# Kernel optimization log

Measured on AMD Instinct MI355X. Metric: run time of the kernel, lower is better.

Reference implementation:

```python
import jax, jax.numpy as jnp
import numpy as np

N, D, H, K, P = 1536, 1024, 16, 64, 8
FREQ_DIM = 14 * 3 * 128  # freq_embedding(pos, 128) flattened


def freq_embedding(t, size):
    # min_freq=0.01, max_freq=2**8 as in the block's call sites
    nf = size // 2
    freqs = (2.0 ** jnp.linspace(np.log2(0.01), np.log2(256.0), nf)).astype(jnp.float32)
    r = t[..., None] * freqs
    return jnp.stack((jnp.sin(r), jnp.cos(r)), axis=-1).reshape(t.shape[0], -1)


def layer_norm(x, eps=1e-5):
    m = jnp.mean(x, -1, keepdims=True)
    v = jnp.var(x, -1, keepdims=True)
    return (x - m) * jax.lax.rsqrt(v + eps)


def cond_norm(x, cond, ws, bs, wb, bb):
    return jax.nn.sigmoid(cond @ ws + bs) * layer_norm(x) + (cond @ wb + bb)


def _unit(v):
    return v * jax.lax.rsqrt(jnp.sum(v * v, -1, keepdims=True) + 1e-8)


def aa_frames(pos):
    # Gram-Schmidt frame from backbone N/CA/C (atom14 slots 0,1,2)
    n, ca, c = pos[:, 0], pos[:, 1], pos[:, 2]
    e1 = _unit(c - ca)
    v2 = n - ca
    e2 = _unit(v2 - jnp.sum(e1 * v2, -1, keepdims=True) * e1)
    e3 = jnp.cross(e1, e2)
    R = jnp.stack([e1, e2, e3], axis=-1)  # [N,3,3]
    return R, ca


def setup_inputs():
    key = jax.random.key(0)
    ks = iter(jax.random.split(key, 64))
    r = lambda *s: jax.random.normal(next(ks), s, jnp.float32)
    w = lambda *s: 0.02 * jax.random.normal(next(ks), s, jnp.float32)
    z = lambda *s: jnp.zeros(s, jnp.float32)
    return dict(
        local=r(N, D), pos=r(N, 14, 3), condition=r(N, D),
        mask=jnp.ones((N,), bool), pair_bias=r(H, N, N),
        w_f1=w(FREQ_DIM, 2 * D), b_f1=z(2 * D), w_f2=w(2 * D, D), b_f2=z(D),
        cn1_ws=w(D, D), cn1_bs=z(D), cn1_wb=w(D, D), cn1_bb=z(D),
        wq=w(D, H * K), wk=w(D, H * K), wv=w(D, H * K),
        wqp=w(D, H * P * 3), wkp=w(D, H * P * 3), wvp=w(D, H * P * 3),
        gamma=z(H), wo=w(H * (K + 4 * P), D), bo=z(D),
        cn2_ws=w(D, D), cn2_bs=z(D), cn2_wb=w(D, D), cn2_bb=z(D),
        wg1=w(D, 2 * D), bg1=z(2 * D), wg2=w(D, 2 * D), bg2=z(2 * D),
        wg3=w(2 * D, D), bg3=z(D),
        cn3_ws=w(D, D), cn3_bs=z(D), cn3_wb=w(D, D), cn3_bb=z(D),
        w_vel=w(D, 14 * 3),
    )


def reference(local, pos, condition, mask, pair_bias,
              w_f1, b_f1, w_f2, b_f2,
              cn1_ws, cn1_bs, cn1_wb, cn1_bb,
              wq, wk, wv, wqp, wkp, wvp, gamma, wo, bo,
              cn2_ws, cn2_bs, cn2_wb, cn2_bb,
              wg1, bg1, wg2, bg2, wg3, bg3,
              cn3_ws, cn3_bs, cn3_wb, cn3_bb, w_vel):
    n = local.shape[0]
    # embed_pred_pos: MLP over freq embedding of coords
    emb = freq_embedding(pos, 128)  # [N, 5376]
    local = local + (jax.nn.silu(emb @ w_f1 + b_f1) @ w_f2 + b_f2)
    # attention branch
    ai = cond_norm(local, condition, cn1_ws, cn1_bs, cn1_wb, cn1_bb)
    R, t = aa_frames(pos)
    q = (ai @ wq).reshape(n, H, K)
    k = (ai @ wk).reshape(n, H, K)
    v = (ai @ wv).reshape(n, H, K)
    to_glob = lambda p: jnp.einsum('nab,nhpb->nhpa', R, p) + t[:, None, None, :]
    qg = to_glob((ai @ wqp).reshape(n, H, P, 3))
    kg = to_glob((ai @ wkp).reshape(n, H, P, 3))
    vg = to_glob((ai @ wvp).reshape(n, H, P, 3))
    qk = jnp.einsum('ihk,jhk->hij', q, k) / np.sqrt(K).astype(np.float32)
    # squared point distances via norm expansion (never materialize [H,N,N,P,3])
    ptdot = jnp.einsum('ihpc,jhpc->hij', qg, kg)
    qn = jnp.sum(qg * qg, axis=(-1, -2)).T  # [H,N]
    kn = jnp.sum(kg * kg, axis=(-1, -2)).T
    dist2 = qn[:, :, None] + kn[None if False else slice(None), None, :] - 2.0 * ptdot
    wc = np.sqrt(2.0 / (9.0 * P)).astype(np.float32)
    logits = qk + pair_bias - 0.5 * wc * jax.nn.softplus(gamma)[:, None, None] * dist2
    logits = jnp.where(mask[None, None, :], logits, -1e9)
    a = jax.nn.softmax(logits, axis=-1)  # [H,N,N]
    o = jnp.einsum('hij,jhk->ihk', a, v).reshape(n, H * K)
    opg = jnp.einsum('hij,jhpc->ihpc', a, vg)
    opl = jnp.einsum('nba,nhpb->nhpa', R, opg - t[:, None, None, :])
    onorm = jnp.sqrt(jnp.sum(opl * opl, -1) + 1e-8).reshape(n, -1)
    upd = jnp.concatenate([o, opl.reshape(n, -1), onorm], axis=-1) @ wo + bo
    local = local + upd
    # gated MLP branch
    x = cond_norm(local, condition, cn2_ws, cn2_bs, cn2_wb, cn2_bb)
    local = local + (jax.nn.silu(x @ wg1 + bg1) * (x @ wg2 + bg2)) @ wg3 + bg3
    # output heads
    ln = cond_norm(local, condition, cn3_ws, cn3_bs, cn3_wb, cn3_bb)
    velocity = (ln @ w_vel).reshape(n, 14, 3)
    return local, velocity
```

## Files before the change

### kernel.cpp

```cpp
#include <hip/hip_runtime.h>
#include <hip/hip_bf16.h>
#include <math.h>

#define NRES 1536
#define NH 16
#define NNF 2359296ull
#define LOG2E 1.44269504f
#define KVS 4
#define LDQ 4224
#define NTPJ 19

typedef unsigned short u16;
typedef __attribute__((ext_vector_type(8))) short short8;
typedef __attribute__((ext_vector_type(4))) unsigned short u16x4;
typedef __attribute__((ext_vector_type(4))) float f32x4;

typedef const __attribute__((address_space(1))) void gvoid;
typedef __attribute__((address_space(3))) void lvoid;

__device__ __forceinline__ u16 f2b(float x){
    __hip_bfloat16 h = __float2bfloat16(x);
    return *reinterpret_cast<u16*>(&h);
}
__device__ __forceinline__ float b2f(u16 u){
    unsigned v = ((unsigned)u) << 16;
    return __uint_as_float(v);
}

#define F_BIAS  1
#define F_SILU  2
#define F_RESID 8
#define F_OUTBF 16

template<int TNF>
__global__ __launch_bounds__(256) void gemm_t(
    const u16* __restrict__ A, int lda, size_t zsA,
    const u16* __restrict__ BT, int ldb, size_t zsB,
    float* __restrict__ Cf, u16* __restrict__ Cb, int ldc, size_t zsC,
    const float* __restrict__ bias, size_t zsBias,
    const float* __restrict__ resid, int ldr, size_t zsR,
    int Ncols, int Kd, int flags, int ksl)
{
    constexpr int TN = TNF * 32;
    __shared__ u16 As[2][128 * 64];
    __shared__ u16 Bs[2][TN * 64];

    unsigned gx = gridDim.x, gy = gridDim.y;
    unsigned nb = gx * gy * gridDim.z;
    unsigned bid = (blockIdx.z * gy + blockIdx.y) * gx + blockIdx.x;
    if ((nb & 7u) == 0u) bid = (bid & 7u) * (nb >> 3) + (bid >> 3);
    const int bxi = bid % gx;
    const int byi = (bid / gx) % gy;
    const int bz  = bid / (gx * gy);

    const int tid = threadIdx.x;
    const int l = tid & 63, w = tid >> 6;
    const int bm = byi * 128, bn = bxi * TN;

    A  += zsA * bz;
    BT += zsB * bz;

    const int kbeg = ksl ? bz * ksl : 0;
    const int kend = ksl ? kbeg + ksl : Kd;
    const int nk = (kend - kbeg) >> 6;

    const int arow   = l >> 3;
    const int aslot  = l & 7;
    const int srcslt = aslot ^ arow;

    const u16* aBase[4];
    const u16* bBase[TN / 32];
    #pragma unroll
    for (int t = 0; t < 4; ++t) {
        int ra = bm + (w * 4 + t) * 8 + arow;
        aBase[t] = A + (size_t)ra * lda + srcslt * 8;
    }
    #pragma unroll
    for (int t = 0; t < TN / 32; ++t) {
        int rb = bn + (w * (TN / 32) + t) * 8 + arow;
        if (rb > Ncols - 1) rb = Ncols - 1;
        bBase[t] = BT + (size_t)rb * ldb + srcslt * 8;
    }

    const int wr = w >> 1, wc = w & 1;
    const int fr = l & 15;
    const int fq = l >> 4;

    f32x4 acc[4][TNF];
    #pragma unroll
    for (int i = 0; i < 4; ++i)
        #pragma unroll
        for (int j = 0; j < TNF; ++j) acc[i][j] = (f32x4){0.f, 0.f, 0.f, 0.f};

    auto stage = [&](int buf, int k0) {
        #pragma unroll
        for (int t = 0; t < 4; ++t)
            __builtin_amdgcn_global_load_lds((gvoid*)(aBase[t] + k0),
                (lvoid*)((char*)As[buf] + (w * 4 + t) * 1024), 16, 0, 0);
        #pragma unroll
        for (int t = 0; t < TN / 32; ++t)
            __builtin_amdgcn_global_load_lds((gvoid*)(bBase[t] + k0),
                (lvoid*)((char*)Bs[buf] + (w * (TN / 32) + t) * 1024), 16, 0, 0);
    };

    stage(0, kbeg);
    __syncthreads();
    int cur = 0;

    for (int it = 0; it < nk; ++it) {
        if (it + 1 < nk) stage(cur ^ 1, kbeg + (it + 1) * 64);
        #pragma unroll
        for (int kk = 0; kk < 2; ++kk) {
            const int slotR = ((kk * 4) + fq) ^ (l & 7);
            short8 av[4], bv[TNF];
            #pragma unroll
            for (int m = 0; m < 4; ++m) {
                int r = wr * 64 + m * 16 + fr;
                av[m] = *(const short8*)((const char*)As[cur] + r * 128 + slotR * 16);
            }
            #pragma unroll
            for (int n = 0; n < TNF; ++n) {
                int r = wc * (TNF * 16) + n * 16 + fr;
                bv[n] = *(const short8*)((const char*)Bs[cur] + r * 128 + slotR * 16);
            }
            #pragma unroll
            for (int m = 0; m < 4; ++m)
                #pragma unroll
                for (int n = 0; n < TNF; ++n)
                    acc[m][n] = __builtin_amdgcn_mfma_f32_16x16x32_bf16(av[m], bv[n], acc[m][n], 0, 0, 0);
        }
        __syncthreads();
        cur ^= 1;
    }

    const float* residz = (flags & F_RESID) ? resid + zsR * bz : nullptr;
    const float* biasz  = (flags & F_BIAS)  ? bias + zsBias * bz : nullptr;
    float* cfz = Cf ? Cf + zsC * bz : nullptr;
    u16*   cbz = Cb ? Cb + zsC * bz : nullptr;

    #pragma unroll
    for (int m = 0; m < 4; ++m) {
        #pragma unroll
        for (int n = 0; n < TNF; ++n) {
            int gc = bn + wc * (TNF * 16) + n * 16 + fr;
            if (gc >= Ncols) continue;
            int gr0 = bm + wr * 64 + m * 16 + fq * 4;
            #pragma unroll
            for (int r = 0; r < 4; ++r) {
                int gr = gr0 + r;
                float v = acc[m][n][r];
                if (flags & F_BIAS)  v += biasz[gc];
                if (flags & F_SILU)  v = v / (1.f + expf(-v));
                if (flags & F_RESID) v += residz[(size_t)gr * ldr + gc];
                if (flags & F_OUTBF) cbz[(size_t)gr * ldc + gc] = f2b(v);
                else                 cfz[(size_t)gr * ldc + gc] = v;
            }
        }
    }
}

__global__ __launch_bounds__(256) void reduce_epi(
    const u16* __restrict__ part, size_t slice, int nsl,
    float* __restrict__ Cf, u16* __restrict__ Cb,
    const float* __restrict__ bias,
    const float* __restrict__ resid, int ldr,
    int M, int Ncols, int flags)
{
    if ((Ncols & 7) == 0) {
        size_t total8 = (size_t)M * Ncols / 8;
        for (size_t i8 = (size_t)blockIdx.x * 256 + threadIdx.x; i8 < total8;
             i8 += (size_t)gridDim.x * 256) {
            size_t i0 = i8 * 8;
            int r = (int)(i0 / (unsigned)Ncols);
            int c0 = (int)(i0 - (size_t)r * Ncols);
            float v[8] = {0,0,0,0,0,0,0,0};
            for (int s = 0; s < nsl; ++s) {
                const u16x4* p = (const u16x4*)(part + (size_t)s * slice + i0);
                u16x4 a = p[0], b = p[1];
                v[0] += b2f(a.x); v[1] += b2f(a.y); v[2] += b2f(a.z); v[3] += b2f(a.w);
                v[4] += b2f(b.x); v[5] += b2f(b.y); v[6] += b2f(b.z); v[7] += b2f(b.w);
            }
            #pragma unroll
            for (int j = 0; j < 8; ++j) {
                if (flags & F_BIAS) v[j] += bias[c0 + j];
                if (flags & F_SILU) v[j] = v[j] / (1.f + expf(-v[j]));
            }
            if (flags & F_RESID) {
                const float4* rp = (const float4*)(resid + (size_t)r * ldr + c0);
                float4 r0 = rp[0], r1 = rp[1];
                v[0] += r0.x; v[1] += r0.y; v[2] += r0.z; v[3] += r0.w;
                v[4] += r1.x; v[5] += r1.y; v[6] += r1.z; v[7] += r1.w;
            }
            if (flags & F_OUTBF) {
                short8 o;
                #pragma unroll
                for (int j = 0; j < 8; ++j) o[j] = (short)f2b(v[j]);
                *(short8*)(Cb + i0) = o;
            } else {
                float4 o0 = {v[0], v[1], v[2], v[3]}, o1 = {v[4], v[5], v[6], v[7]};
                float4* cp = (float4*)(Cf + i0);
                cp[0] = o0; cp[1] = o1;
            }
        }
    } else {
        size_t total = (size_t)M * Ncols;
        for (size_t i = (size_t)blockIdx.x * 256 + threadIdx.x; i < total;
             i += (size_t)gridDim.x * 256) {
            float v = 0.f;
            for (int s = 0; s < nsl; ++s) v += b2f(part[(size_t)s * slice + i]);
            if (flags & F_OUTBF) Cb[i] = f2b(v);
            else                 Cf[i] = v;
        }
    }
}

__global__ __launch_bounds__(256) void reduce_cn(
    const u16* __restrict__ part, size_t slice, int nsl,
    const float* __restrict__ bias, const float* __restrict__ resid,
    float* __restrict__ locOut,
    const u16* __restrict__ cs, const u16* __restrict__ cb,
    u16* __restrict__ normB)
{
    int row = blockIdx.x, tid = threadIdx.x;
    size_t base = (size_t)row * 1024 + tid * 4;
    float v[4];
    {
        float4 rv = *(const float4*)(resid + base);
        v[0] = rv.x; v[1] = rv.y; v[2] = rv.z; v[3] = rv.w;
    }
    for (int s = 0; s < nsl; ++s) {
        u16x4 p = *(const u16x4*)(part + (size_t)s * slice + base);
        v[0] += b2f(p.x); v[1] += b2f(p.y); v[2] += b2f(p.z); v[3] += b2f(p.w);
    }
    {
        float4 bv = *(const float4*)(bias + tid * 4);
        v[0] += bv.x; v[1] += bv.y; v[2] += bv.z; v[3] += bv.w;
    }
    *(float4*)(locOut + base) = (float4){v[0], v[1], v[2], v[3]};

    float s1 = v[0] + v[1] + v[2] + v[3];
    float s2 = v[0]*v[0] + v[1]*v[1] + v[2]*v[2] + v[3]*v[3];
    __shared__ float r1[256], r2[256];
    r1[tid] = s1; r2[tid] = s2;
    __syncthreads();
    for (int st = 128; st > 0; st >>= 1) {
        if (tid < st) { r1[tid] += r1[tid + st]; r2[tid] += r2[tid + st]; }
        __syncthreads();
    }
    float mean = r1[0] * (1.f / 1024.f);
    float var = r2[0] * (1.f / 1024.f) - mean * mean;
    float rs = rsqrtf(var + 1e-5f);
    u16x4 sv = *(const u16x4*)(cs + base);
    u16x4 bv = *(const u16x4*)(cb + base);
    u16x4 o;
    o.x = f2b((1.f / (1.f + expf(-b2f(sv.x)))) * (v[0] - mean) * rs + b2f(bv.x));
    o.y = f2b((1.f / (1.f + expf(-b2f(sv.y)))) * (v[1] - mean) * rs + b2f(bv.y));
    o.z = f2b((1.f / (1.f + expf(-b2f(sv.z)))) * (v[2] - mean) * rs + b2f(bv.z));
    o.w = f2b((1.f / (1.f + expf(-b2f(sv.w)))) * (v[3] - mean) * rs + b2f(bv.w));
    *(u16x4*)(normB + base) = o;
}

__global__ __launch_bounds__(256, 2) void attn_kernel(
    const u16* __restrict__ qe, const u16* __restrict__ ke,
    const u16* __restrict__ vt, const float* __restrict__ pb,
    u16* __restrict__ Opart, float* __restrict__ mlpart)
{
    __shared__ u16 Ks[2][64 * 128];
    __shared__ u16 Vs[2][96 * 64];
    __shared__ u16 Ps[64 * 64];

    unsigned gx = gridDim.x, gy = gridDim.y;
    unsigned nb = gx * gy * gridDim.z;
    unsigned bid = (blockIdx.z * gy + blockIdx.y) * gx + blockIdx.x;
    bid = (bid & 7u) * (nb >> 3) + (bid >> 3);
    const int qx = bid % gx;
    const int h  = (bid / gx) % gy;
    const int z  = bid / (gx * gy);

    const int tid = threadIdx.x;
    const int l = tid & 63, w = tid >> 6;
    const int q0 = qx * 64;
    const int fr = l & 15, fq = l >> 4;

    const u16* keh = ke + (size_t)h * NRES * 128;
    const u16* vth = vt + (size_t)h * 96 * NRES;

    const int kr4 = l >> 4, ks16 = l & 15;
    const int vr8 = l >> 3, vs8 = l & 7;

    short8 qv[4];
    {
        const u16* qrow = qe + ((size_t)h * NRES + (q0 + w * 16 + fr)) * 128 + fq * 8;
        #pragma unroll
        for (int kk = 0; kk < 4; ++kk)
            qv[kk] = *(const short8*)(qrow + kk * 32);
    }

    float m_run[4], l_run[4];
    f32x4 oacc[6];
    #pragma unroll
    for (int r = 0; r < 4; ++r) { m_run[r] = -1e30f; l_run[r] = 0.f; }
    #pragma unroll
    for (int n = 0; n < 6; ++n) oacc[n] = (f32x4){0.f, 0.f, 0.f, 0.f};

    const int NIT = NRES / 64 / KVS;
    const int jbase = z * (NRES / KVS);
    int cur = 0;

    auto stage = [&](int buf, int j0) {
        #pragma unroll
        for (int t = 0; t < 4; ++t) {
            int row = w * 16 + t * 4 + kr4;
            int ss = ks16 ^ (row & 7);
            __builtin_amdgcn_global_load_lds(
                (gvoid*)(keh + (size_t)(j0 + row) * 128 + ss * 8),
                (lvoid*)((char*)Ks[buf] + (w * 16 + t * 4) * 256), 16, 0, 0);
        }
        #pragma unroll
        for (int t = 0; t < 3; ++t) {
            int row = w * 24 + t * 8 + vr8;
            int ss = vs8 ^ (row & 7);
            __builtin_amdgcn_global_load_lds(
                (gvoid*)(vth + (size_t)row * NRES + j0 + ss * 8),
                (lvoid*)((char*)Vs[buf] + (w * 24 + t * 8) * 128), 16, 0, 0);
        }
    };
    const float* pbrow = pb + ((size_t)h * NRES + (q0 + w * 16 + fq * 4)) * NRES + fr;

    f32x4 pbv[4], pbn[4] = {};
    stage(0, jbase);
    #pragma unroll
    for (int n = 0; n < 4; ++n)
        #pragma unroll
        for (int r = 0; r < 4; ++r)
            pbv[n][r] = pbrow[(size_t)r * NRES + jbase + n * 16];
    __syncthreads();

    for (int it = 0; it < NIT; ++it) {
        if (it + 1 < NIT) {
            int j1 = jbase + (it + 1) * 64;
            stage(cur ^ 1, j1);
            #pragma unroll
            for (int n = 0; n < 4; ++n)
                #pragma unroll
                for (int r = 0; r < 4; ++r)
                    pbn[n][r] = pbrow[(size_t)r * NRES + j1 + n * 16];
        }

        f32x4 sacc[4];
        #pragma unroll
        for (int n = 0; n < 4; ++n) sacc[n] = (f32x4){0.f, 0.f, 0.f, 0.f};
        __builtin_amdgcn_s_setprio(1);
        #pragma unroll
        for (int kk = 0; kk < 4; ++kk) {
            #pragma unroll
            for (int n = 0; n < 4; ++n) {
                int row = n * 16 + fr;
                short8 bv = *(const short8*)((const char*)Ks[cur] + row * 256
                                             + (((kk * 4 + fq) ^ (fr & 7)) * 16));
                sacc[n] = __builtin_amdgcn_mfma_f32_16x16x32_bf16(qv[kk], bv, sacc[n], 0, 0, 0);
            }
        }
        __builtin_amdgcn_s_setprio(0);
        #pragma unroll
        for (int n = 0; n < 4; ++n) sacc[n] += pbv[n];

        float alpha[4];
        #pragma unroll
        for (int r = 0; r < 4; ++r) {
            float v = fmaxf(fmaxf(sacc[0][r], sacc[1][r]), fmaxf(sacc[2][r], sacc[3][r]));
            v = fmaxf(v, __shfl_xor(v, 1, 64));
            v = fmaxf(v, __shfl_xor(v, 2, 64));
            v = fmaxf(v, __shfl_xor(v, 4, 64));
            v = fmaxf(v, __shfl_xor(v, 8, 64));
            float mn = fmaxf(m_run[r], v);
            alpha[r] = exp2f((m_run[r] - mn) * LOG2E);
            m_run[r] = mn;
        }

        float psum[4] = {0.f, 0.f, 0.f, 0.f};
        #pragma unroll
        for (int n = 0; n < 4; ++n) {
            int col = n * 16 + fr;
            #pragma unroll
            for (int r = 0; r < 4; ++r) {
                float p = exp2f((sacc[n][r] - m_run[r]) * LOG2E);
                psum[r] += p;
                int rowf = w * 16 + fq * 4 + r;
                int byte = rowf * 128 + (((col >> 3) ^ (rowf & 7)) * 16) + (col & 7) * 2;
                *(u16*)((char*)Ps + byte) = f2b(p);
            }
        }
        #pragma unroll
        for (int r = 0; r < 4; ++r) {
            float v = psum[r];
            v += __shfl_xor(v, 1, 64);
            v += __shfl_xor(v, 2, 64);
            v += __shfl_xor(v, 4, 64);
            v += __shfl_xor(v, 8, 64);
            l_run[r] = l_run[r] * alpha[r] + v;
        }
        #pragma unroll
        for (int n = 0; n < 6; ++n)
            #pragma unroll
            for (int r = 0; r < 4; ++r)
                oacc[n][r] *= alpha[r];

        __builtin_amdgcn_s_setprio(1);
        #pragma unroll
        for (int kk = 0; kk < 2; ++kk) {
            int prow = w * 16 + fr;
            short8 pa = *(const short8*)((const char*)Ps + prow * 128
                                         + (((kk * 4 + fq) ^ (prow & 7)) * 16));
            #pragma unroll
            for (int n = 0; n < 6; ++n) {
                int vrow = n * 16 + fr;
                short8 vv = *(const short8*)((const char*)Vs[cur] + vrow * 128
                                             + (((kk * 4 + fq) ^ (fr & 7)) * 16));
                oacc[n] = __builtin_amdgcn_mfma_f32_16x16x32_bf16(pa, vv, oacc[n], 0, 0, 0);
            }
        }
        __builtin_amdgcn_s_setprio(0);

        __syncthreads();
        cur ^= 1;
        #pragma unroll
        for (int n = 0; n < 4; ++n) pbv[n] = pbn[n];
    }

    u16* Oz = Opart + ((size_t)z * NH + h) * NRES * 96;
    #pragma unroll
    for (int n = 0; n < 6; ++n) {
        int c = n * 16 + fr;
        #pragma unroll
        for (int r = 0; r < 4; ++r) {
            int row = q0 + w * 16 + fq * 4 + r;
            Oz[(size_t)row * 96 + c] = f2b(oacc[n][r]);
        }
    }
    if (fr == 0) {
        float* mlz = mlpart + ((size_t)z * NH + h) * NRES * 2;
        #pragma unroll
        for (int r = 0; r < 4; ++r) {
            int row = q0 + w * 16 + fq * 4 + r;
            mlz[row * 2 + 0] = m_run[r];
            mlz[row * 2 + 1] = l_run[r];
        }
    }
}

__global__ __launch_bounds__(256) void combine_fin(
    const u16* __restrict__ Opart, const float* __restrict__ mlpart,
    const float* __restrict__ Rb, const float* __restrict__ tb,
    u16* __restrict__ featB)
{
    int idx = blockIdx.x * 256 + threadIdx.x;
    if (idx >= NRES * NH) return;
    int n = idx >> 4, h = idx & 15;

    float m[KVS], lv[KVS], wgt[KVS];
    float mm = -1e30f;
    #pragma unroll
    for (int s = 0; s < KVS; ++s) {
        size_t rr = ((size_t)s * NH + h) * NRES + n;
        m[s] = mlpart[rr * 2];
        lv[s] = mlpart[rr * 2 + 1];
        mm = fmaxf(mm, m[s]);
    }
    float ll = 0.f;
    #pragma unroll
    for (int s = 0; s < KVS; ++s) {
        wgt[s] = exp2f((m[s] - mm) * LOG2E);
        ll += lv[s] * wgt[s];
    }
    float inv = 1.f / ll;
    const u16* op[KVS];
    #pragma unroll
    for (int s = 0; s < KVS; ++s)
        op[s] = Opart + (((size_t)s * NH + h) * NRES + n) * 96;

    u16* fb = featB + (size_t)n * 1536;
    #pragma unroll
    for (int k = 0; k < 64; ++k) {
        float v = 0.f;
        #pragma unroll
        for (int s = 0; s < KVS; ++s) v += b2f(op[s][k]) * wgt[s];
        fb[h * 64 + k] = f2b(v * inv);
    }

    float R[9];
    #pragma unroll
    for (int a = 0; a < 9; ++a) R[a] = Rb[(size_t)n * 9 + a];
    float t0 = tb[(size_t)n * 3 + 0], t1 = tb[(size_t)n * 3 + 1], t2 = tb[(size_t)n * 3 + 2];
    #pragma unroll
    for (int p = 0; p < 8; ++p) {
        float d[3];
        #pragma unroll
        for (int dd = 0; dd < 3; ++dd) {
            int c = 64 + p * 3 + dd;
            float v = 0.f;
            #pragma unroll
            for (int s = 0; s < KVS; ++s) v += b2f(op[s][c]) * wgt[s];
            d[dd] = v * inv;
        }
        float x = d[0] - t0, y = d[1] - t1, z = d[2] - t2;
        float a0 = R[0] * x + R[3] * y + R[6] * z;
        float a1 = R[1] * x + R[4] * y + R[7] * z;
        float a2 = R[2] * x + R[5] * y + R[8] * z;
        fb[1024 + h * 24 + p * 3 + 0] = f2b(a0);
        fb[1024 + h * 24 + p * 3 + 1] = f2b(a1);
        fb[1024 + h * 24 + p * 3 + 2] = f2b(a2);
        fb[1408 + h * 8 + p] = f2b(sqrtf(a0 * a0 + a1 * a1 + a2 * a2 + 1e-8f));
    }
}

struct TpMega {
    const float* src[NTPJ];
    u16* dst[NTPJ];
    int ldi[NTPJ], ldo[NTPJ], K[NTPJ], N[NTPJ];
    int bx[NTPJ], start[NTPJ];
};

__global__ __launch_bounds__(256) void transpose_mega(TpMega J)
{
    __shared__ float t[32][33];
    int b = blockIdx.x;
    int j = NTPJ - 1;
    while (J.start[j] > b) --j;
    int lb = b - J.start[j];
    int bxn = J.bx[j];
    int n0 = (lb % bxn) * 32;
    int k0 = (lb / bxn) * 32;
    const float* in = J.src[j];
    u16* out = J.dst[j];
    int ldi = J.ldi[j], ldo = J.ldo[j], Kk = J.K[j], Nn = J.N[j];
    int tx = threadIdx.x & 31, ty = threadIdx.x >> 5;
    #pragma unroll
    for (int jj = 0; jj < 4; ++jj) {
        int k = k0 + ty + jj * 8;
        if (k < Kk && n0 + tx < Nn) t[ty + jj * 8][tx] = in[(size_t)k * ldi + n0 + tx];
    }
    __syncthreads();
    #pragma unroll
    for (int jj = 0; jj < 4; ++jj) {
        int n = n0 + ty + jj * 8;
        int k = k0 + tx;
        if (n < Nn && k < Kk) out[(size_t)n * ldo + k] = f2b(t[tx][ty + jj * 8]);
    }
}

__global__ __launch_bounds__(256) void vt_pack(
    const float* __restrict__ qkc, const float* __restrict__ vgt,
    u16* __restrict__ vt)
{
    __shared__ float t[32][33];
    int h = blockIdx.z, grp = blockIdx.y, n0 = blockIdx.x * 32;
    int tx = threadIdx.x & 31, ty = threadIdx.x >> 5;
    #pragma unroll
    for (int j = 0; j < 4; ++j) {
        int n = n0 + ty + j * 8;
        int c = grp * 32 + tx;
        float v = 0.f;
        if (c < 64) v = qkc[(size_t)n * LDQ + 2048 + h * 64 + c];
        else if (c < 88) v = vgt[(size_t)n * 384 + h * 24 + (c - 64)];
        t[ty + j * 8][tx] = v;
    }
    __syncthreads();
    #pragma unroll
    for (int j = 0; j < 4; ++j) {
        int r = grp * 32 + ty + j * 8;
        vt[((size_t)h * 96 + r) * NRES + n0 + tx] = f2b(t[tx][ty + j * 8]);
    }
}

__global__ __launch_bounds__(256) void prologue_kernel(
    const float* __restrict__ pos, const float* __restrict__ cond,
    const float* __restrict__ cn1_bs, const float* __restrict__ cn1_bb,
    const float* __restrict__ cn2_bs, const float* __restrict__ cn2_bb,
    const float* __restrict__ cn3_bs, const float* __restrict__ cn3_bb,
    const float* __restrict__ bg1, const float* __restrict__ bg2,
    float* __restrict__ Rb, float* __restrict__ tb,
    u16* __restrict__ emb, u16* __restrict__ condB,
    float* __restrict__ bias2, float* __restrict__ biasg)
{
    int b = blockIdx.x, tid = threadIdx.x;
    if (b < 16128) {
        int idx = b * 256 + tid;
        int f = idx & 63;
        int rest = idx >> 6;
        int coord = rest % 42;
        int n = rest / 42;
        float t = pos[(size_t)n * 42 + coord];
        const double l0 = -6.643856189774724;
        const double step = 14.643856189774724 / 63.0;
        float freq = exp2f((float)(l0 + f * step));
        float r = t * freq;
        size_t o = (size_t)n * 5376 + (size_t)coord * 128 + 2 * f;
        emb[o]     = f2b(sinf(r));
        emb[o + 1] = f2b(cosf(r));
    } else if (b < 16896) {
        int i = (b - 16128) * 256 + tid;
        size_t i0 = (size_t)i * 8;
        const float4* p = (const float4*)(cond + i0);
        float4 a = p[0], bb = p[1];
        short8 o;
        o[0]=(short)f2b(a.x); o[1]=(short)f2b(a.y); o[2]=(short)f2b(a.z); o[3]=(short)f2b(a.w);
        o[4]=(short)f2b(bb.x); o[5]=(short)f2b(bb.y); o[6]=(short)f2b(bb.z); o[7]=(short)f2b(bb.w);
        *(short8*)(condB + i0) = o;
    } else if (b < 16902) {
        int n = (b - 16896) * 256 + tid;
        if (n >= NRES) return;
        const float* p = pos + (size_t)n * 42;
        float nx = p[0], ny = p[1], nz = p[2];
        float cax = p[3], cay = p[4], caz = p[5];
        float cx = p[6], cy = p[7], cz = p[8];
        float v1x = cx - cax, v1y = cy - cay, v1z = cz - caz;
        float i1 = rsqrtf(v1x * v1x + v1y * v1y + v1z * v1z + 1e-8f);
        float e1x = v1x * i1, e1y = v1y * i1, e1z = v1z * i1;
        float v2x = nx - cax, v2y = ny - cay, v2z = nz - caz;
        float d = e1x * v2x + e1y * v2y + e1z * v2z;
        float wx = v2x - d * e1x, wy = v2y - d * e1y, wz = v2z - d * e1z;
        float i2 = rsqrtf(wx * wx + wy * wy + wz * wz + 1e-8f);
        float e2x = wx * i2, e2y = wy * i2, e2z = wz * i2;
        float e3x = e1y * e2z - e1z * e2y;
        float e3y = e1z * e2x - e1x * e2z;
        float e3z = e1x * e2y - e1y * e2x;
        float* R = Rb + (size_t)n * 9;
        R[0] = e1x; R[1] = e2x; R[2] = e3x;
        R[3] = e1y; R[4] = e2y; R[5] = e3y;
        R[6] = e1z; R[7] = e2z; R[8] = e3z;
        tb[(size_t)n * 3 + 0] = cax;
        tb[(size_t)n * 3 + 1] = cay;
        tb[(size_t)n * 3 + 2] = caz;
    } else if (b < 16906) {
        int i = (b - 16902) * 256 + tid;
        if (i >= 1024) return;
        bias2[i] = cn1_bs[i]; bias2[1024 + i] = cn1_bb[i]; bias2[2048 + i] = cn2_bs[i];
        bias2[3072 + i] = cn2_bb[i]; bias2[4096 + i] = cn3_bs[i]; bias2[5120 + i] = cn3_bb[i];
    } else {
        int i = (b - 16906) * 256 + tid;
        if (i >= 2048) return;
        biasg[i] = bg1[i]; biasg[2048 + i] = bg2[i];
    }
}

__global__ __launch_bounds__(256) void pack_attn(
    const float* __restrict__ qkc,
    const float* __restrict__ Rb, const float* __restrict__ tb,
    const float* __restrict__ gamma,
    u16* __restrict__ qe, u16* __restrict__ ke, float* __restrict__ vgt)
{
    int b = blockIdx.x;
    if (b < 1536) {
        int idx = b * 256 + threadIdx.x;
        int g = idx & 15;
        int t = idx >> 4;
        int n = t % NRES;
        int h = t / NRES;
        size_t o = ((size_t)h * NRES + n) * 128 + g * 8;
        if (g < 8) {
            const float4* q4 = (const float4*)(qkc + (size_t)n * LDQ + h * 64 + g * 8);
            const float4* k4 = (const float4*)(qkc + (size_t)n * LDQ + 1024 + h * 64 + g * 8);
            float4 qa = q4[0], qb2 = q4[1], ka = k4[0], kb2 = k4[1];
            short8 oq, ok;
            oq[0]=(short)f2b(0.125f*qa.x); oq[1]=(short)f2b(0.125f*qa.y);
            oq[2]=(short)f2b(0.125f*qa.z); oq[3]=(short)f2b(0.125f*qa.w);
            oq[4]=(short)f2b(0.125f*qb2.x); oq[5]=(short)f2b(0.125f*qb2.y);
            oq[6]=(short)f2b(0.125f*qb2.z); oq[7]=(short)f2b(0.125f*qb2.w);
            ok[0]=(short)f2b(ka.x); ok[1]=(short)f2b(ka.y); ok[2]=(short)f2b(ka.z); ok[3]=(short)f2b(ka.w);
            ok[4]=(short)f2b(kb2.x); ok[5]=(short)f2b(kb2.y); ok[6]=(short)f2b(kb2.z); ok[7]=(short)f2b(kb2.w);
            *(short8*)(qe + o) = oq;
            *(short8*)(ke + o) = ok;
        } else if (g >= 11) {
            short8 zz = {};
            *(short8*)(qe + o) = zz;
            *(short8*)(ke + o) = zz;
        }
        return;
    }
    int idx = (b - 1536) * 256 + threadIdx.x;
    if (idx >= NRES * NH) return;
    int n = idx >> 4, h = idx & 15;
    float R[9];
    #pragma unroll
    for (int a = 0; a < 9; ++a) R[a] = Rb[(size_t)n * 9 + a];
    float t0 = tb[(size_t)n * 3 + 0], t1 = tb[(size_t)n * 3 + 1], t2 = tb[(size_t)n * 3 + 2];
    float g = gamma[h];
    float sp = (g > 20.f) ? g : log1pf(expf(g));
    float ch = 0.5f * (1.f / 6.f) * sp;

    u16* qeh = qe + ((size_t)h * NRES + n) * 128;
    u16* keh = ke + ((size_t)h * NRES + n) * 128;
    const float* qp = qkc + (size_t)n * LDQ + 3072 + h * 24;
    const float* kp = qkc + (size_t)n * LDQ + 3456 + h * 24;
    const float* vp = qkc + (size_t)n * LDQ + 3840 + h * 24;
    float kn = 0.f;
    #pragma unroll
    for (int p = 0; p < 8; ++p) {
        {
            float x = qp[p*3], y = qp[p*3+1], z = qp[p*3+2];
            float g0 = R[0] * x + R[1] * y + R[2] * z + t0;
            float g1 = R[3] * x + R[4] * y + R[5] * z + t1;
            float g2 = R[6] * x + R[7] * y + R[8] * z + t2;
            qeh[64 + p * 3 + 0] = f2b(2.f * ch * g0);
            qeh[64 + p * 3 + 1] = f2b(2.f * ch * g1);
            qeh[64 + p * 3 + 2] = f2b(2.f * ch * g2);
        }
        {
            float x = kp[p*3], y = kp[p*3+1], z = kp[p*3+2];
            float g0 = R[0] * x + R[1] * y + R[2] * z + t0;
            float g1 = R[3] * x + R[4] * y + R[5] * z + t1;
            float g2 = R[6] * x + R[7] * y + R[8] * z + t2;
            keh[64 + p * 3 + 0] = f2b(g0);
            keh[64 + p * 3 + 1] = f2b(g1);
            keh[64 + p * 3 + 2] = f2b(g2);
            kn += g0 * g0 + g1 * g1 + g2 * g2;
        }
        {
            float x = vp[p*3], y = vp[p*3+1], z = vp[p*3+2];
            vgt[(size_t)n * 384 + h * 24 + p * 3 + 0] = R[0] * x + R[1] * y + R[2] * z + t0;
            vgt[(size_t)n * 384 + h * 24 + p * 3 + 1] = R[3] * x + R[4] * y + R[5] * z + t1;
            vgt[(size_t)n * 384 + h * 24 + p * 3 + 2] = R[6] * x + R[7] * y + R[8] * z + t2;
        }
    }
    qeh[88] = f2b(1.0f);
    keh[88] = f2b(-ch * kn);
}

__global__ __launch_bounds__(256) void glu_kernel(const u16* __restrict__ g12, u16* __restrict__ gm)
{
    int i = blockIdx.x * 256 + threadIdx.x;
    if (i >= NRES * 2048 / 8) return;
    size_t i0 = (size_t)i * 8;
    short8 a8 = *(const short8*)(g12 + i0);
    short8 b8 = *(const short8*)(g12 + (size_t)NRES * 2048 + i0);
    short8 o;
    #pragma unroll
    for (int j = 0; j < 8; ++j) {
        float a = b2f((u16)a8[j]);
        float b = b2f((u16)b8[j]);
        float s = a / (1.f + expf(-a));
        o[j] = (short)f2b(s * b);
    }
    *(short8*)(gm + i0) = o;
}

extern "C" void kernel_launch(void* const* d_in, const int* in_sizes, int n_in,
                              void* d_out, int out_size, void* d_ws, size_t ws_size,
                              hipStream_t stream)
{
    const float* local_in = (const float*)d_in[0];
    const float* pos      = (const float*)d_in[1];
    const float* cond     = (const float*)d_in[2];
    const float* pb       = (const float*)d_in[4];
    const float* w_f1     = (const float*)d_in[5];
    const float* b_f1     = (const float*)d_in[6];
    const float* w_f2     = (const float*)d_in[7];
    const float* b_f2     = (const float*)d_in[8];
    const float* cn1_ws   = (const float*)d_in[9];
    const float* cn1_bs   = (const float*)d_in[10];
    const float* cn1_wb   = (const float*)d_in[11];
    const float* cn1_bb   = (const float*)d_in[12];
    const float* wq       = (const float*)d_in[13];
    const float* wk       = (const float*)d_in[14];
    const float* wv       = (const float*)d_in[15];
    const float* wqp      = (const float*)d_in[16];
    const float* wkp      = (const float*)d_in[17];
    const float* wvp      = (const float*)d_in[18];
    const float* gamma    = (const float*)d_in[19];
    const float* wo       = (const float*)d_in[20];
    const float* bo       = (const float*)d_in[21];
    const float* cn2_ws   = (const float*)d_in[22];
    const float* cn2_bs   = (const float*)d_in[23];
    const float* cn2_wb   = (const float*)d_in[24];
    const float* cn2_bb   = (const float*)d_in[25];
    const float* wg1      = (const float*)d_in[26];
    const float* bg1      = (const float*)d_in[27];
    const float* wg2      = (const float*)d_in[28];
    const float* bg2      = (const float*)d_in[29];
    const float* wg3      = (const float*)d_in[30];
    const float* bg3      = (const float*)d_in[31];
    const float* cn3_ws   = (const float*)d_in[32];
    const float* cn3_bs   = (const float*)d_in[33];
    const float* cn3_wb   = (const float*)d_in[34];
    const float* cn3_bb   = (const float*)d_in[35];
    const float* w_vel    = (const float*)d_in[36];

    float* out = (float*)d_out;
    float* ws  = (float*)d_ws;

    size_t off = 0;
    auto alloc = [&](size_t nf) -> float* { float* p = ws + off; off += (nf + 7) & ~7ull; return p; };

    const size_t NN1 = (size_t)NRES * 1024;
    float* Rb    = alloc(NRES * 9);
    float* tb    = alloc(NRES * 3);
    float* loc   = alloc(NN1);
    u16*   cs6b  = (u16*)alloc(6 * NN1 / 2);
    u16*   condB = (u16*)alloc(NN1 / 2);
    u16*   normB = (u16*)alloc(NN1 / 2);
    float* bias2 = alloc(6 * 1024);
    float* biasg = alloc(2 * 2048);
    float* qkc   = alloc((size_t)NRES * LDQ);
    float* vgt   = alloc((size_t)NRES * 384);
    u16*   qeB   = (u16*)alloc((size_t)NH * NRES * 128 / 2);
    u16*   keB   = (u16*)alloc((size_t)NH * NRES * 128 / 2);
    u16*   vTB   = (u16*)alloc((size_t)NH * 96 * NRES / 2);
    u16*   featB = (u16*)alloc((size_t)NRES * 1536 / 2);
    u16*   g1sB  = (u16*)alloc((size_t)NRES * 2048 / 2);
    u16*   gmB   = (u16*)alloc((size_t)NRES * 2048 / 2);
    u16*   cnT9  = (u16*)alloc((size_t)9 * 1024 * 1024 / 2);
    u16*   ptsT  = (u16*)alloc((size_t)3 * 384 * 1024 / 2);
    u16*   wgT   = (u16*)alloc((size_t)2 * 2048 * 1024 / 2);
    u16*   wf1T  = (u16*)alloc((size_t)2048 * 5376 / 2);
    u16*   wf2T  = (u16*)alloc((size_t)1024 * 2048 / 2);
    u16*   woT   = (u16*)alloc((size_t)1024 * 1536 / 2);
    u16*   wg3T  = (u16*)alloc((size_t)1024 * 2048 / 2);
    u16*   wvT   = (u16*)alloc((size_t)42 * 1024 / 2 + 8);
    u16*   embB  = (u16*)alloc((size_t)NRES * 5376 / 2);
    u16*   hidB  = (u16*)alloc((size_t)NRES * 2048 / 2);
    u16*   pscr  = (u16*)alloc((size_t)2 * NRES * 2048 * 4 / 2);
    u16*   Opart = (u16*)alloc((size_t)KVS * NH * NRES * 96 / 2);
    float* mlprt = alloc((size_t)KVS * NH * NRES * 2);

    const float* nilf = nullptr;

    auto gemm = [&](int tnf, const u16* A, int lda, size_t zsA,
                    const u16* BT, int ldb, size_t zsB,
                    float* Cf, u16* Cb2, int ldc, size_t zsC,
                    const float* bias, size_t zsBias,
                    const float* resid, int ldr, size_t zsR,
                    int Nc, int Kd, int flags, int gz, int ksl) {
        int tn = tnf * 32;
        dim3 grid((Nc + tn - 1) / tn, NRES / 128, gz);
        if (tnf == 4)
            hipLaunchKernelGGL(gemm_t<4>, grid, dim3(256), 0, stream,
                               A, lda, zsA, BT, ldb, zsB, Cf, Cb2, ldc, zsC,
                               bias, zsBias, resid, ldr, zsR, Nc, Kd, flags, ksl);
        else
            hipLaunchKernelGGL(gemm_t<2>, grid, dim3(256), 0, stream,
                               A, lda, zsA, BT, ldb, zsB, Cf, Cb2, ldc, zsC,
                               bias, zsBias, resid, ldr, zsR, Nc, Kd, flags, ksl);
    };
    auto red = [&](const u16* part, size_t slice, int nsl, float* Cf, u16* Cb2,
                   const float* bias, const float* resid, int ldr, int Nc, int flags) {
        hipLaunchKernelGGL(reduce_epi, dim3(1024), dim3(256), 0, stream,
                           part, slice, nsl, Cf, Cb2, bias, resid, ldr, NRES, Nc, flags);
    };
    auto redcn = [&](const u16* part, size_t slice, int nsl,
                     const float* bias, const float* resid, float* locOut, int cnIdx) {
        hipLaunchKernelGGL(reduce_cn, dim3(NRES), dim3(256), 0, stream,
                           part, slice, nsl, bias, resid, locOut,
                           cs6b + (size_t)(2 * cnIdx) * NN1,
                           cs6b + (size_t)(2 * cnIdx + 1) * NN1, normB);
    };

    hipLaunchKernelGGL(prologue_kernel, dim3(16914), dim3(256), 0, stream,
                       pos, cond, cn1_bs, cn1_bb, cn2_bs, cn2_bb, cn3_bs, cn3_bb,
                       bg1, bg2, Rb, tb, embB, condB, bias2, biasg);

    {
        TpMega J;
        int jn = 0, start = 0;
        auto addJob = [&](const float* src, u16* dst, int ldi, int ldo, int K, int N) {
            J.src[jn] = src; J.dst[jn] = dst;
            J.ldi[jn] = ldi; J.ldo[jn] = ldo; J.K[jn] = K; J.N[jn] = N;
            int bx = (N + 31) / 32, by = (K + 31) / 32;
            J.bx[jn] = bx; J.start[jn] = start;
            start += bx * by;
            ++jn;
        };
        const float* cn6[6] = {cn1_ws, cn1_wb, cn2_ws, cn2_wb, cn3_ws, cn3_wb};
        for (int i = 0; i < 6; ++i)
            addJob(cn6[i], cnT9 + (size_t)i * 1024 * 1024, 1024, 1024, 1024, 1024);
        addJob(wq, cnT9 + (size_t)6 * 1024 * 1024, 1024, 1024, 1024, 1024);
        addJob(wk, cnT9 + (size_t)7 * 1024 * 1024, 1024, 1024, 1024, 1024);
        addJob(wv, cnT9 + (size_t)8 * 1024 * 1024, 1024, 1024, 1024, 1024);
        addJob(wqp, ptsT,                        384, 1024, 1024, 384);
        addJob(wkp, ptsT + (size_t)384 * 1024,   384, 1024, 1024, 384);
        addJob(wvp, ptsT + (size_t)2 * 384 * 1024, 384, 1024, 1024, 384);
        addJob(wg1, wgT,                        2048, 1024, 1024, 2048);
        addJob(wg2, wgT + (size_t)2048 * 1024,  2048, 1024, 1024, 2048);
        addJob(w_f1, wf1T, 2048, 5376, 5376, 2048);
        addJob(w_f2, wf2T, 1024, 2048, 2048, 1024);
        addJob(wo,   woT,  1024, 1536, 1536, 1024);
        addJob(wg3,  wg3T, 1024, 2048, 2048, 1024);
        addJob(w_vel, wvT,   42, 1024, 1024, 42);
        hipLaunchKernelGGL(transpose_mega, dim3(start), dim3(256), 0, stream, J);
    }

    gemm(2, condB, 1024, 0, cnT9, 1024, (size_t)1024 * 1024, nullptr, cs6b, 1024, NN1,
         bias2, 1024, nilf, 0, 0, 1024, 1024, F_BIAS | F_OUTBF, 6, 0);

    gemm(2, embB, 5376, 0, wf1T, 5376, 0, nullptr, pscr, 2048, (size_t)NRES * 2048,
         nilf, 0, nilf, 0, 0, 2048, 5376, F_OUTBF, 4, 1344);
    red(pscr, (size_t)NRES * 2048, 4, nullptr, hidB, b_f1, nilf, 0,
        2048, F_BIAS | F_SILU | F_OUTBF);
    gemm(2, hidB, 2048, 0, wf2T, 2048, 0, nullptr, pscr, 1024, NN1,
         nilf, 0, nilf, 0, 0, 1024, 2048, F_OUTBF, 4, 512);
    redcn(pscr, NN1, 4, b_f2, local_in, loc, 0);

    gemm(2, normB, 1024, 0, cnT9 + (size_t)6 * 1024 * 1024, 1024, 0,
         qkc, nullptr, LDQ, 0, nilf, 0, nilf, 0, 0, LDQ, 1024, 0, 1, 0);

    hipLaunchKernelGGL(pack_attn, dim3(1536 + 96), dim3(256), 0, stream,
                       qkc, Rb, tb, gamma, qeB, keB, vgt);
    hipLaunchKernelGGL(vt_pack, dim3(NRES / 32, 3, NH), dim3(256), 0, stream,
                       qkc, vgt, vTB);

    hipLaunchKernelGGL(attn_kernel, dim3(NRES / 64, NH, KVS), dim3(256), 0, stream,
                       qeB, keB, vTB, pb, Opart, mlprt);
    hipLaunchKernelGGL(combine_fin, dim3(96), dim3(256), 0, stream,
                       Opart, mlprt, Rb, tb, featB);

    gemm(2, featB, 1536, 0, woT, 1536, 0, nullptr, pscr, 1024, NN1,
         nilf, 0, nilf, 0, 0, 1024, 1536, F_OUTBF, 4, 384);
    redcn(pscr, NN1, 4, bo, loc, loc, 1);

    gemm(2, normB, 1024, 0, wgT, 1024, (size_t)2048 * 1024, nullptr, g1sB, 2048, (size_t)NRES * 2048,
         biasg, 2048, nilf, 0, 0, 2048, 1024, F_BIAS | F_OUTBF, 2, 0);
    u16* gmO = embB;
    hipLaunchKernelGGL(glu_kernel, dim3((NRES * 2048 / 8 + 255) / 256), dim3(256), 0, stream, g1sB, gmO);
    gemm(2, gmO, 2048, 0, wg3T, 2048, 0, nullptr, pscr, 1024, NN1,
         nilf, 0, nilf, 0, 0, 1024, 2048, F_OUTBF, 4, 512);
    redcn(pscr, NN1, 4, bg3, loc, out, 2);

    gemm(2, normB, 1024, 0, wvT, 1024, 0, nullptr, pscr, 42, (size_t)NRES * 42,
         nilf, 0, nilf, 0, 0, 42, 1024, F_OUTBF, 8, 128);
    red(pscr, (size_t)NRES * 42, 8, out + (size_t)NRES * 1024, nullptr,
        nilf, nilf, 0, 42, 0);
}
```

Measured before the change: 464.7 us.

## Merge prologue with weight transposes and batch two independent GEMMs in one launch

Folds the weight-transpose blocks into the prologue kernel as extra blocks, and replaces two back-to-back GEMM launches (condition-projection GEMM and split-K freq-embedding GEMM) with a single dual-job GEMM kernel that dispatches blocks by index. This removes launch gaps and tail underutilization between small independent kernels so their blocks can co-schedule. The dual kernel uses a fixed 128x64 tile and its own block swizzle, which may differ in efficiency from the original templated gemm. The shared-memory tile is now allocated for every prologue block, which may reduce occupancy of the embedding blocks.

```diff
diff --git a/kernel.cpp b/kernel.cpp
--- a/kernel.cpp
+++ b/kernel.cpp
@@ -9,6 +9,7 @@
 #define KVS 4
 #define LDQ 4224
 #define NTPJ 19
+#define PROBLK 16914
 
 typedef unsigned short u16;
 typedef __attribute__((ext_vector_type(8))) short short8;
@@ -154,6 +155,130 @@
                 if (flags & F_RESID) v += residz[(size_t)gr * ldr + gc];
                 if (flags & F_OUTBF) cbz[(size_t)gr * ldc + gc] = f2b(v);
                 else                 cfz[(size_t)gr * ldc + gc] = v;
+            }
+        }
+    }
+}
+
+struct GJob {
+    const u16* A;
+    const u16* BT;
+    u16* C;
+    const float* bias;
+    int lda, ldb, ldc;
+    size_t zsA, zsB, zsC, zsBias;
+    int Nc, Kd, ksl, flags;
+    unsigned gx, gy, start, nb;
+};
+
+__global__ __launch_bounds__(256) void gemm_dual(GJob j0, GJob j1)
+{
+    __shared__ u16 As[2][128 * 64];
+    __shared__ u16 Bs[2][64 * 64];
+
+    GJob J = (blockIdx.x >= j1.start) ? j1 : j0;
+    unsigned bid = blockIdx.x - J.start;
+    if ((J.nb & 7u) == 0u) bid = (bid & 7u) * (J.nb >> 3) + (bid >> 3);
+    const int bxi = bid % J.gx;
+    const int byi = (bid / J.gx) % J.gy;
+    const int bz  = bid / (J.gx * J.gy);
+
+    const int tid = threadIdx.x;
+    const int l = tid & 63, w = tid >> 6;
+    const int bm = byi * 128, bn = bxi * 64;
+
+    const u16* A  = J.A + J.zsA * bz;
+    const u16* BT = J.BT + J.zsB * bz;
+
+    const int kbeg = J.ksl ? bz * J.ksl : 0;
+    const int kend = J.ksl ? kbeg + J.ksl : J.Kd;
+    const int nk = (kend - kbeg) >> 6;
+
+    const int arow   = l >> 3;
+    const int aslot  = l & 7;
+    const int srcslt = aslot ^ arow;
+
+    const u16* aBase[4];
+    const u16* bBase[2];
+    #pragma unroll
+    for (int t = 0; t < 4; ++t) {
+        int ra = bm + (w * 4 + t) * 8 + arow;
+        aBase[t] = A + (size_t)ra * J.lda + srcslt * 8;
+    }
+    #pragma unroll
+    for (int t = 0; t < 2; ++t) {
+        int rb = bn + (w * 2 + t) * 8 + arow;
+        if (rb > J.Nc - 1) rb = J.Nc - 1;
+        bBase[t] = BT + (size_t)rb * J.ldb + srcslt * 8;
+    }
+
+    const int wr = w >> 1, wc = w & 1;
+    const int fr = l & 15;
+    const int fq = l >> 4;
+
+    f32x4 acc[4][2];
+    #pragma unroll
+    for (int i = 0; i < 4; ++i)
+        #pragma unroll
+        for (int j = 0; j < 2; ++j) acc[i][j] = (f32x4){0.f, 0.f, 0.f, 0.f};
+
+    auto stage = [&](int buf, int k0) {
+        #pragma unroll
+        for (int t = 0; t < 4; ++t)
+            __builtin_amdgcn_global_load_lds((gvoid*)(aBase[t] + k0),
+                (lvoid*)((char*)As[buf] + (w * 4 + t) * 1024), 16, 0, 0);
+        #pragma unroll
+        for (int t = 0; t < 2; ++t)
+            __builtin_amdgcn_global_load_lds((gvoid*)(bBase[t] + k0),
+                (lvoid*)((char*)Bs[buf] + (w * 2 + t) * 1024), 16, 0, 0);
+    };
+
+    stage(0, kbeg);
+    __syncthreads();
+    int cur = 0;
+
+    for (int it = 0; it < nk; ++it) {
+        if (it + 1 < nk) stage(cur ^ 1, kbeg + (it + 1) * 64);
+        #pragma unroll
+        for (int kk = 0; kk < 2; ++kk) {
+            const int slotR = ((kk * 4) + fq) ^ (l & 7);
+            short8 av[4], bv[2];
+            #pragma unroll
+            for (int m = 0; m < 4; ++m) {
+                int r = wr * 64 + m * 16 + fr;
+                av[m] = *(const short8*)((const char*)As[cur] + r * 128 + slotR * 16);
+            }
+            #pragma unroll
+            for (int n = 0; n < 2; ++n) {
+                int r = wc * 32 + n * 16 + fr;
+                bv[n] = *(const short8*)((const char*)Bs[cur] + r * 128 + slotR * 16);
+            }
+            #pragma unroll
+            for (int m = 0; m < 4; ++m)
+                #pragma unroll
+                for (int n = 0; n < 2; ++n)
+                    acc[m][n] = __builtin_amdgcn_mfma_f32_16x16x32_bf16(av[m], bv[n], acc[m][n], 0, 0, 0);
+        }
+        __syncthreads();
+        cur ^= 1;
+    }
+
+    const float* biasz = (J.flags & F_BIAS) ? J.bias + J.zsBias * bz : nullptr;
+    u16* cbz = J.C + J.zsC * bz;
+
+    #pragma unroll
+    for (int m = 0; m < 4; ++m) {
+        #pragma unroll
+        for (int n = 0; n < 2; ++n) {
+            int gc = bn + wc * 32 + n * 16 + fr;
+            if (gc >= J.Nc) continue;
+            int gr0 = bm + wr * 64 + m * 16 + fq * 4;
+            #pragma unroll
+            for (int r = 0; r < 4; ++r) {
+                int gr = gr0 + r;
+                float v = acc[m][n][r];
+                if (J.flags & F_BIAS) v += biasz[gc];
+                cbz[(size_t)gr * J.ldc + gc] = f2b(v);
             }
         }
     }
@@ -521,59 +646,7 @@
     int bx[NTPJ], start[NTPJ];
 };
 
-__global__ __launch_bounds__(256) void transpose_mega(TpMega J)
-{
-    __shared__ float t[32][33];
-    int b = blockIdx.x;
-    int j = NTPJ - 1;
-    while (J.start[j] > b) --j;
-    int lb = b - J.start[j];
-    int bxn = J.bx[j];
-    int n0 = (lb % bxn) * 32;
-    int k0 = (lb / bxn) * 32;
-    const float* in = J.src[j];
-    u16* out = J.dst[j];
-    int ldi = J.ldi[j], ldo = J.ldo[j], Kk = J.K[j], Nn = J.N[j];
-    int tx = threadIdx.x & 31, ty = threadIdx.x >> 5;
-    #pragma unroll
-    for (int jj = 0; jj < 4; ++jj) {
-        int k = k0 + ty + jj * 8;
-        if (k < Kk && n0 + tx < Nn) t[ty + jj * 8][tx] = in[(size_t)k * ldi + n0 + tx];
-    }
-    __syncthreads();
-    #pragma unroll
-    for (int jj = 0; jj < 4; ++jj) {
-        int n = n0 + ty + jj * 8;
-        int k = k0 + tx;
-        if (n < Nn && k < Kk) out[(size_t)n * ldo + k] = f2b(t[tx][ty + jj * 8]);
-    }
-}
-
-__global__ __launch_bounds__(256) void vt_pack(
-    const float* __restrict__ qkc, const float* __restrict__ vgt,
-    u16* __restrict__ vt)
-{
-    __shared__ float t[32][33];
-    int h = blockIdx.z, grp = blockIdx.y, n0 = blockIdx.x * 32;
-    int tx = threadIdx.x & 31, ty = threadIdx.x >> 5;
-    #pragma unroll
-    for (int j = 0; j < 4; ++j) {
-        int n = n0 + ty + j * 8;
-        int c = grp * 32 + tx;
-        float v = 0.f;
-        if (c < 64) v = qkc[(size_t)n * LDQ + 2048 + h * 64 + c];
-        else if (c < 88) v = vgt[(size_t)n * 384 + h * 24 + (c - 64)];
-        t[ty + j * 8][tx] = v;
-    }
-    __syncthreads();
-    #pragma unroll
-    for (int j = 0; j < 4; ++j) {
-        int r = grp * 32 + ty + j * 8;
-        vt[((size_t)h * 96 + r) * NRES + n0 + tx] = f2b(t[tx][ty + j * 8]);
-    }
-}
-
-__global__ __launch_bounds__(256) void prologue_kernel(
+__global__ __launch_bounds__(256) void prep_kernel(
     const float* __restrict__ pos, const float* __restrict__ cond,
     const float* __restrict__ cn1_bs, const float* __restrict__ cn1_bb,
     const float* __restrict__ cn2_bs, const float* __restrict__ cn2_bb,
@@ -581,20 +654,48 @@
     const float* __restrict__ bg1, const float* __restrict__ bg2,
     float* __restrict__ Rb, float* __restrict__ tb,
     u16* __restrict__ emb, u16* __restrict__ condB,
-    float* __restrict__ bias2, float* __restrict__ biasg)
+    float* __restrict__ bias2, float* __restrict__ biasg,
+    TpMega J)
 {
+    __shared__ float t[32][33];
     int b = blockIdx.x, tid = threadIdx.x;
+    if (b >= PROBLK) {
+        int tb2 = b - PROBLK;
+        int j = NTPJ - 1;
+        while (J.start[j] > tb2) --j;
+        int lb = tb2 - J.start[j];
+        int bxn = J.bx[j];
+        int n0 = (lb % bxn) * 32;
+        int k0 = (lb / bxn) * 32;
+        const float* in = J.src[j];
+        u16* out = J.dst[j];
+        int ldi = J.ldi[j], ldo = J.ldo[j], Kk = J.K[j], Nn = J.N[j];
+        int tx = tid & 31, ty = tid >> 5;
+        #pragma unroll
+        for (int jj = 0; jj < 4; ++jj) {
+            int k = k0 + ty + jj * 8;
+            if (k < Kk && n0 + tx < Nn) t[ty + jj * 8][tx] = in[(size_t)k * ldi + n0 + tx];
+        }
+        __syncthreads();
+        #pragma unroll
+        for (int jj = 0; jj < 4; ++jj) {
+            int n = n0 + ty + jj * 8;
+            int k = k0 + tx;
+            if (n < Nn && k < Kk) out[(size_t)n * ldo + k] = f2b(t[tx][ty + jj * 8]);
+        }
+        return;
+    }
     if (b < 16128) {
         int idx = b * 256 + tid;
         int f = idx & 63;
         int rest = idx >> 6;
         int coord = rest % 42;
         int n = rest / 42;
-        float t = pos[(size_t)n * 42 + coord];
+        float tt = pos[(size_t)n * 42 + coord];
         const double l0 = -6.643856189774724;
         const double step = 14.643856189774724 / 63.0;
         float freq = exp2f((float)(l0 + f * step));
-        float r = t * freq;
+        float r = tt * freq;
         size_t o = (size_t)n * 5376 + (size_t)coord * 128 + 2 * f;
         emb[o]     = f2b(sinf(r));
         emb[o + 1] = f2b(cosf(r));
@@ -644,6 +745,30 @@
     }
 }
 
+__global__ __launch_bounds__(256) void vt_pack(
+    const float* __restrict__ qkc, const float* __restrict__ vgt,
+    u16* __restrict__ vt)
+{
+    __shared__ float t[32][33];
+    int h = blockIdx.z, grp = blockIdx.y, n0 = blockIdx.x * 32;
+    int tx = threadIdx.x & 31, ty = threadIdx.x >> 5;
+    #pragma unroll
+    for (int j = 0; j < 4; ++j) {
+        int n = n0 + ty + j * 8;
+        int c = grp * 32 + tx;
+        float v = 0.f;
+        if (c < 64) v = qkc[(size_t)n * LDQ + 2048 + h * 64 + c];
+        else if (c < 88) v = vgt[(size_t)n * 384 + h * 24 + (c - 64)];
+        t[ty + j * 8][tx] = v;
+    }
+    __syncthreads();
+    #pragma unroll
+    for (int j = 0; j < 4; ++j) {
+        int r = grp * 32 + ty + j * 8;
+        vt[((size_t)h * 96 + r) * NRES + n0 + tx] = f2b(t[tx][ty + j * 8]);
+    }
+}
+
 __global__ __launch_bounds__(256) void pack_attn(
     const float* __restrict__ qkc,
     const float* __restrict__ Rb, const float* __restrict__ tb,
@@ -855,10 +980,6 @@
                            cs6b + (size_t)(2 * cnIdx + 1) * NN1, normB);
     };
 
-    hipLaunchKernelGGL(prologue_kernel, dim3(16914), dim3(256), 0, stream,
-                       pos, cond, cn1_bs, cn1_bb, cn2_bs, cn2_bb, cn3_bs, cn3_bb,
-                       bg1, bg2, Rb, tb, embB, condB, bias2, biasg);
-
     {
         TpMega J;
         int jn = 0, start = 0;
@@ -886,14 +1007,25 @@
         addJob(wo,   woT,  1024, 1536, 1536, 1024);
         addJob(wg3,  wg3T, 1024, 2048, 2048, 1024);
         addJob(w_vel, wvT,   42, 1024, 1024, 42);
-        hipLaunchKernelGGL(transpose_mega, dim3(start), dim3(256), 0, stream, J);
-    }
-
-    gemm(2, condB, 1024, 0, cnT9, 1024, (size_t)1024 * 1024, nullptr, cs6b, 1024, NN1,
-         bias2, 1024, nilf, 0, 0, 1024, 1024, F_BIAS | F_OUTBF, 6, 0);
-
-    gemm(2, embB, 5376, 0, wf1T, 5376, 0, nullptr, pscr, 2048, (size_t)NRES * 2048,
-         nilf, 0, nilf, 0, 0, 2048, 5376, F_OUTBF, 4, 1344);
+        hipLaunchKernelGGL(prep_kernel, dim3(PROBLK + start), dim3(256), 0, stream,
+                           pos, cond, cn1_bs, cn1_bb, cn2_bs, cn2_bb, cn3_bs, cn3_bb,
+                           bg1, bg2, Rb, tb, embB, condB, bias2, biasg, J);
+    }
+
+    {
+        GJob jc, je;
+        jc.A = condB; jc.BT = cnT9; jc.C = cs6b; jc.bias = bias2;
+        jc.lda = 1024; jc.ldb = 1024; jc.ldc = 1024;
+        jc.zsA = 0; jc.zsB = (size_t)1024 * 1024; jc.zsC = NN1; jc.zsBias = 1024;
+        jc.Nc = 1024; jc.Kd = 1024; jc.ksl = 0; jc.flags = F_BIAS;
+        jc.gx = 16; jc.gy = 12; jc.start = 0; jc.nb = 16 * 12 * 6;
+        je.A = embB; je.BT = wf1T; je.C = pscr; je.bias = nullptr;
+        je.lda = 5376; je.ldb = 5376; je.ldc = 2048;
+        je.zsA = 0; je.zsB = 0; je.zsC = (size_t)NRES * 2048; je.zsBias = 0;
+        je.Nc = 2048; je.Kd = 5376; je.ksl = 1344; je.flags = 0;
+        je.gx = 32; je.gy = 12; je.start = jc.nb; je.nb = 32 * 12 * 4;
+        hipLaunchKernelGGL(gemm_dual, dim3(jc.nb + je.nb), dim3(256), 0, stream, jc, je);
+    }
     red(pscr, (size_t)NRES * 2048, 4, nullptr, hidB, b_f1, nilf, 0,
         2048, F_BIAS | F_SILU | F_OUTBF);
     gemm(2, hidB, 2048, 0, wf2T, 2048, 0, nullptr, pscr, 1024, NN1,
```

Measured after the change: 449.4 us. -3.3%, faster.
